# Kernel optimization log

Measured on AMD Instinct MI355X. Metric: run time of the kernel, lower is better.

Reference implementation:

```python
import jax, jax.numpy as jnp
import numpy as np

B = 524288  # batch
NQ = 4      # qubits -> 16-dim state vector


def _rx(t):
    c = jnp.cos(t / 2).astype(jnp.complex64)
    s = (-1j * jnp.sin(t / 2)).astype(jnp.complex64)
    return jnp.stack([jnp.stack([c, s], -1), jnp.stack([s, c], -1)], -2)


def _ry(t):
    c = jnp.cos(t / 2)
    s = jnp.sin(t / 2)
    return jnp.stack([jnp.stack([c, -s], -1), jnp.stack([s, c], -1)], -2).astype(jnp.complex64)


def _rz(t):
    em = jnp.exp(-0.5j * t).astype(jnp.complex64)
    ep = jnp.exp(0.5j * t).astype(jnp.complex64)
    z = jnp.zeros_like(em)
    return jnp.stack([jnp.stack([em, z], -1), jnp.stack([z, ep], -1)], -2)


def _apply(state, U, w):
    # state: [B,2,2,2,2]; wire w lives on axis w+1
    s = jnp.moveaxis(state, w + 1, 1)
    if U.ndim == 3:  # per-sample gate (encoder)
        s = jnp.einsum('bij,bj...->bi...', U, s)
    else:            # shared trainable gate
        s = jnp.einsum('ij,bj...->bi...', U, s)
    return jnp.moveaxis(s, 1, w + 1)


def _cnot(state, c, t):
    s = jnp.moveaxis(state, (c + 1, t + 1), (1, 2))
    s = jnp.stack([s[:, 0], s[:, 1, ::-1]], axis=1)  # flip target where control=1
    return jnp.moveaxis(s, (1, 2), (c + 1, t + 1))


def setup_inputs() -> dict:
    key = jax.random.key(0)
    k1, k2 = jax.random.split(key)
    inputs = jax.random.normal(k1, (B, 4), dtype=jnp.float32)
    theta = jax.random.normal(k2, (16,), dtype=jnp.float32)
    return {"inputs": inputs, "theta": theta}


def reference(inputs, theta):
    b = inputs.shape[0]
    state = jnp.zeros((b, 16), jnp.complex64).at[:, 0].set(1.0)
    state = state.reshape(b, 2, 2, 2, 2)
    # --- encoder: per-sample rotations rx(w0), ry(w1), rz(w2), rx(w3) ---
    state = _apply(state, _rx(inputs[:, 0]), 0)
    state = _apply(state, _ry(inputs[:, 1]), 1)
    state = _apply(state, _rz(inputs[:, 2]), 2)
    state = _apply(state, _rx(inputs[:, 3]), 3)
    # --- trainable 20-op layer (fixed representative sequence) ---
    k = 0
    for q in range(NQ):
        state = _apply(state, _rx(theta[k]), q); k += 1
        state = _apply(state, _ry(theta[k]), q); k += 1
        state = _apply(state, _rz(theta[k]), q); k += 1
    for (c, t) in [(0, 1), (1, 2), (2, 3), (3, 0)]:
        state = _cnot(state, c, t)
    for q in range(NQ):
        state = _apply(state, _rx(theta[k]), q); k += 1
    # --- MeasureAll(PauliZ): <Z_w> per wire ---
    flat = state.reshape(b, 16)
    probs = flat.real ** 2 + flat.imag ** 2  # [B,16]
    bits = (jnp.arange(16)[:, None] >> jnp.arange(NQ - 1, -1, -1)[None, :]) & 1  # [16,4], wire0=MSB
    sign = (1.0 - 2.0 * bits).astype(jnp.float32)
    expz = probs @ sign  # [B,4]
    return expz[:, :, None]  # unsqueeze(-1)
```

## Files before the change

### kernel.cpp

```cpp
#include <hip/hip_runtime.h>
#include <hip/hip_bf16.h>


__global__ __launch_bounds__(256) void qsim_kernel(
        const float* __restrict__ x,
        const float* __restrict__ theta,
        float* __restrict__ out,
        int n) {
    __shared__ __align__(16) float cst[40];
    int tid = threadIdx.x;
    if (tid < 4) {
        int q = tid;
        float a = theta[3*q], bb = theta[3*q+1], c = theta[3*q+2];
        float sa, ca, sb, cb, sc, cc;
        __sincosf(0.5f*a,  &sa, &ca);
        __sincosf(0.5f*bb, &sb, &cb);
        __sincosf(0.5f*c,  &sc, &cc);
        float m00r =  cb*ca, m00i =  sb*sa;
        float m01r = -sb*ca, m01i = -cb*sa;
        float m10r =  sb*ca, m10i = -cb*sa;
        float m11r =  cb*ca, m11i = -sb*sa;
        float* T = cst + 8*q;
        T[0] = cc*m00r + sc*m00i;  T[1] = cc*m00i - sc*m00r;
        T[2] = cc*m01r + sc*m01i;  T[3] = cc*m01i - sc*m01r;
        T[4] = cc*m10r - sc*m10i;  T[5] = cc*m10i + sc*m10r;
        T[6] = cc*m11r - sc*m11i;  T[7] = cc*m11i + sc*m11r;
        float sfq, cfq;
        __sincosf(theta[12+q], &sfq, &cfq);
        cst[32+q] = cfq;
        cst[36+q] = 2.0f*sfq;
    }
    __syncthreads();

    int b = blockIdx.x * 256 + tid;
    if (b >= n) return;

    float4 xv = ((const float4*)x)[b];

    float T[32];
    #pragma unroll
    for (int i = 0; i < 8; ++i) ((float4*)T)[i] = ((const float4*)cst)[i];
    float4 cf  = ((const float4*)cst)[8];
    float4 sf2 = ((const float4*)cst)[9];

    float s0 = __sinf(0.5f*xv.x), c0 = __cosf(0.5f*xv.x);
    float s1 = __sinf(0.5f*xv.y), c1 = __cosf(0.5f*xv.y);
    float s2 = __sinf(0.5f*xv.z), c2 = __cosf(0.5f*xv.z);
    float s3 = __sinf(0.5f*xv.w), c3 = __cosf(0.5f*xv.w);

    float var[4], vai[4], vbr[4], vbi[4];
    {
        const float* t = T + 0;
        var[0] = t[0]*c0 + t[3]*s0;  vai[0] = t[1]*c0 - t[2]*s0;
        vbr[0] = t[4]*c0 + t[7]*s0;  vbi[0] = t[5]*c0 - t[6]*s0;
    }
    {
        const float* t = T + 8;
        var[1] = t[0]*c1 + t[2]*s1;  vai[1] = t[1]*c1 + t[3]*s1;
        vbr[1] = t[4]*c1 + t[6]*s1;  vbi[1] = t[5]*c1 + t[7]*s1;
    }
    {
        const float* t = T + 16;
        var[2] = t[0]*c2 + t[1]*s2;  vai[2] = t[1]*c2 - t[0]*s2;
        vbr[2] = t[4]*c2 + t[5]*s2;  vbi[2] = t[5]*c2 - t[4]*s2;
    }
    {
        const float* t = T + 24;
        var[3] = t[0]*c3 + t[3]*s3;  vai[3] = t[1]*c3 - t[2]*s3;
        vbr[3] = t[4]*c3 + t[7]*s3;  vbi[3] = t[5]*c3 - t[6]*s3;
    }

    float u01r[4], u01i[4], u23r[4], u23i[4];
    #pragma unroll
    for (int i0 = 0; i0 < 2; ++i0) {
        float ar = i0 ? vbr[0] : var[0], ai = i0 ? vbi[0] : vai[0];
        #pragma unroll
        for (int i1 = 0; i1 < 2; ++i1) {
            float br = i1 ? vbr[1] : var[1], bi = i1 ? vbi[1] : vai[1];
            u01r[2*i0+i1] = ar*br - ai*bi;
            u01i[2*i0+i1] = ar*bi + ai*br;
        }
    }
    #pragma unroll
    for (int i2 = 0; i2 < 2; ++i2) {
        float ar = i2 ? vbr[2] : var[2], ai = i2 ? vbi[2] : vai[2];
        #pragma unroll
        for (int i3 = 0; i3 < 2; ++i3) {
            float br = i3 ? vbr[3] : var[3], bi = i3 ? vbi[3] : vai[3];
            u23r[2*i2+i3] = ar*br - ai*bi;
            u23i[2*i2+i3] = ar*bi + ai*br;
        }
    }
    float pr[16], pi[16];
    #pragma unroll
    for (int h = 0; h < 4; ++h)
        #pragma unroll
        for (int l = 0; l < 4; ++l) {
            pr[4*h+l] = u01r[h]*u23r[l] - u01i[h]*u23i[l];
            pi[4*h+l] = u01r[h]*u23i[l] + u01i[h]*u23r[l];
        }

    #define SWP(A,Bq) { float t_; t_=pr[A]; pr[A]=pr[Bq]; pr[Bq]=t_; \
                        t_=pi[A]; pi[A]=pi[Bq]; pi[Bq]=t_; }
    SWP(8,12)  SWP(9,13)  SWP(10,14) SWP(11,15)
    SWP(4,6)   SWP(5,7)   SWP(12,14) SWP(13,15)
    SWP(2,3)   SWP(6,7)   SWP(10,11) SWP(14,15)
    SWP(1,9)   SWP(3,11)  SWP(5,13)  SWP(7,15)
    #undef SWP

    float d[16];
    #pragma unroll
    for (int i = 0; i < 16; ++i) d[i] = pr[i]*pr[i] + pi[i]*pi[i];

    float s1a[8], d1[8];
    #pragma unroll
    for (int k = 0; k < 8; ++k) { s1a[k] = d[2*k]+d[2*k+1]; d1[k] = d[2*k]-d[2*k+1]; }
    float z3 = ((d1[0]+d1[1])+(d1[2]+d1[3])) + ((d1[4]+d1[5])+(d1[6]+d1[7]));
    float s2a[4], d2[4];
    #pragma unroll
    for (int k = 0; k < 4; ++k) { s2a[k] = s1a[2*k]+s1a[2*k+1]; d2[k] = s1a[2*k]-s1a[2*k+1]; }
    float z2 = (d2[0]+d2[1]) + (d2[2]+d2[3]);
    float s3a[2], d3[2];
    #pragma unroll
    for (int k = 0; k < 2; ++k) { s3a[k] = s2a[2*k]+s2a[2*k+1]; d3[k] = s2a[2*k]-s2a[2*k+1]; }
    float z1 = d3[0] + d3[1];
    float z0 = s3a[0] - s3a[1];

    float y[4];
    #pragma unroll
    for (int w = 0; w < 4; ++w) {
        int m = 8 >> w;
        float acc = 0.f;
        #pragma unroll
        for (int i = 0; i < 16; ++i)
            if (!(i & m)) acc += pr[i]*pi[i+m] - pi[i]*pr[i+m];
        y[w] = acc;
    }

    float4 o;
    o.x = cf.x*z0 + sf2.x*y[0];
    o.y = cf.y*z1 + sf2.y*y[1];
    o.z = cf.z*z2 + sf2.z*y[2];
    o.w = cf.w*z3 + sf2.w*y[3];
    ((float4*)out)[b] = o;
}

extern "C" void kernel_launch(void* const* d_in, const int* in_sizes, int n_in,
                              void* d_out, int out_size, void* d_ws, size_t ws_size,
                              hipStream_t stream) {
    const float* inputs = (const float*)d_in[0];
    const float* theta  = (const float*)d_in[1];
    float* out = (float*)d_out;
    int n = in_sizes[0] / 4;
    int blocks = (n + 255) / 256;
    qsim_kernel<<<blocks, 256, 0, stream>>>(inputs, theta, out, n);
}
```

Measured before the change: 67.22 us.

## Compute expectations analytically from per-qubit product-state Bloch components

```diff
diff --git a/kernel.cpp b/kernel.cpp
--- a/kernel.cpp
+++ b/kernel.cpp
@@ -1,5 +1,4 @@
 #include <hip/hip_runtime.h>
-#include <hip/hip_bf16.h>
 
 
 __global__ __launch_bounds__(256) void qsim_kernel(
@@ -20,15 +19,15 @@
         float m01r = -sb*ca, m01i = -cb*sa;
         float m10r =  sb*ca, m10i = -cb*sa;
         float m11r =  cb*ca, m11i = -sb*sa;
-        float* T = cst + 8*q;
-        T[0] = cc*m00r + sc*m00i;  T[1] = cc*m00i - sc*m00r;
-        T[2] = cc*m01r + sc*m01i;  T[3] = cc*m01i - sc*m01r;
-        T[4] = cc*m10r - sc*m10i;  T[5] = cc*m10i + sc*m10r;
-        T[6] = cc*m11r - sc*m11i;  T[7] = cc*m11i + sc*m11r;
+        float* Tq = cst + 8*q;
+        Tq[0] = cc*m00r + sc*m00i;  Tq[1] = cc*m00i - sc*m00r;
+        Tq[2] = cc*m01r + sc*m01i;  Tq[3] = cc*m01i - sc*m01r;
+        Tq[4] = cc*m10r - sc*m10i;  Tq[5] = cc*m10i + sc*m10r;
+        Tq[6] = cc*m11r - sc*m11i;  Tq[7] = cc*m11i + sc*m11r;
         float sfq, cfq;
         __sincosf(theta[12+q], &sfq, &cfq);
         cst[32+q] = cfq;
-        cst[36+q] = 2.0f*sfq;
+        cst[36+q] = (q == 3 ? -8.0f : 4.0f) * sfq;
     }
     __syncthreads();
 
@@ -40,8 +39,8 @@
     float T[32];
     #pragma unroll
     for (int i = 0; i < 8; ++i) ((float4*)T)[i] = ((const float4*)cst)[i];
-    float4 cf  = ((const float4*)cst)[8];
-    float4 sf2 = ((const float4*)cst)[9];
+    float4 cf = ((const float4*)cst)[8];
+    float4 sf = ((const float4*)cst)[9];
 
     float s0 = __sinf(0.5f*xv.x), c0 = __cosf(0.5f*xv.x);
     float s1 = __sinf(0.5f*xv.y), c1 = __cosf(0.5f*xv.y);
@@ -70,78 +69,23 @@
         vbr[3] = t[4]*c3 + t[7]*s3;  vbi[3] = t[5]*c3 - t[6]*s3;
     }
 
-    float u01r[4], u01i[4], u23r[4], u23i[4];
-    #pragma unroll
-    for (int i0 = 0; i0 < 2; ++i0) {
-        float ar = i0 ? vbr[0] : var[0], ai = i0 ? vbi[0] : vai[0];
-        #pragma unroll
-        for (int i1 = 0; i1 < 2; ++i1) {
-            float br = i1 ? vbr[1] : var[1], bi = i1 ? vbi[1] : vai[1];
-            u01r[2*i0+i1] = ar*br - ai*bi;
-            u01i[2*i0+i1] = ar*bi + ai*br;
-        }
-    }
-    #pragma unroll
-    for (int i2 = 0; i2 < 2; ++i2) {
-        float ar = i2 ? vbr[2] : var[2], ai = i2 ? vbi[2] : vai[2];
-        #pragma unroll
-        for (int i3 = 0; i3 < 2; ++i3) {
-            float br = i3 ? vbr[3] : var[3], bi = i3 ? vbi[3] : vai[3];
-            u23r[2*i2+i3] = ar*br - ai*bi;
-            u23i[2*i2+i3] = ar*bi + ai*br;
-        }
-    }
-    float pr[16], pi[16];
-    #pragma unroll
-    for (int h = 0; h < 4; ++h)
-        #pragma unroll
-        for (int l = 0; l < 4; ++l) {
-            pr[4*h+l] = u01r[h]*u23r[l] - u01i[h]*u23i[l];
-            pi[4*h+l] = u01r[h]*u23i[l] + u01i[h]*u23r[l];
-        }
-
-    #define SWP(A,Bq) { float t_; t_=pr[A]; pr[A]=pr[Bq]; pr[Bq]=t_; \
-                        t_=pi[A]; pi[A]=pi[Bq]; pi[Bq]=t_; }
-    SWP(8,12)  SWP(9,13)  SWP(10,14) SWP(11,15)
-    SWP(4,6)   SWP(5,7)   SWP(12,14) SWP(13,15)
-    SWP(2,3)   SWP(6,7)   SWP(10,11) SWP(14,15)
-    SWP(1,9)   SWP(3,11)  SWP(5,13)  SWP(7,15)
-    #undef SWP
-
-    float d[16];
-    #pragma unroll
-    for (int i = 0; i < 16; ++i) d[i] = pr[i]*pr[i] + pi[i]*pi[i];
-
-    float s1a[8], d1[8];
-    #pragma unroll
-    for (int k = 0; k < 8; ++k) { s1a[k] = d[2*k]+d[2*k+1]; d1[k] = d[2*k]-d[2*k+1]; }
-    float z3 = ((d1[0]+d1[1])+(d1[2]+d1[3])) + ((d1[4]+d1[5])+(d1[6]+d1[7]));
-    float s2a[4], d2[4];
-    #pragma unroll
-    for (int k = 0; k < 4; ++k) { s2a[k] = s1a[2*k]+s1a[2*k+1]; d2[k] = s1a[2*k]-s1a[2*k+1]; }
-    float z2 = (d2[0]+d2[1]) + (d2[2]+d2[3]);
-    float s3a[2], d3[2];
-    #pragma unroll
-    for (int k = 0; k < 2; ++k) { s3a[k] = s2a[2*k]+s2a[2*k+1]; d3[k] = s2a[2*k]-s2a[2*k+1]; }
-    float z1 = d3[0] + d3[1];
-    float z0 = s3a[0] - s3a[1];
-
-    float y[4];
+    float zq[4], Xq[4], Yq[4];
     #pragma unroll
     for (int w = 0; w < 4; ++w) {
-        int m = 8 >> w;
-        float acc = 0.f;
-        #pragma unroll
-        for (int i = 0; i < 16; ++i)
-            if (!(i & m)) acc += pr[i]*pi[i+m] - pi[i]*pr[i+m];
-        y[w] = acc;
+        float p0 = var[w]*var[w] + vai[w]*vai[w];
+        float p1 = vbr[w]*vbr[w] + vbi[w]*vbi[w];
+        zq[w] = p0 - p1;
+        Xq[w] = var[w]*vbr[w] + vai[w]*vbi[w];
+        Yq[w] = var[w]*vbi[w] - vai[w]*vbr[w];
     }
 
+    float z01 = zq[0]*zq[1];
+    float z23 = zq[2]*zq[3];
     float4 o;
-    o.x = cf.x*z0 + sf2.x*y[0];
-    o.y = cf.y*z1 + sf2.y*y[1];
-    o.z = cf.z*z2 + sf2.z*y[2];
-    o.w = cf.w*z3 + sf2.w*y[3];
+    o.x = (cf.x*zq[1] + sf.x*(Xq[0]*Yq[1])) * z23;
+    o.y = (cf.y*zq[1] + sf.y*(Yq[1]*Xq[2])) * zq[0];
+    o.z = (cf.z*zq[2] + sf.z*(Yq[2]*Xq[3])) * z01;
+    o.w = cf.w*(z01*z23) + sf.w*((Yq[0]*Yq[1])*(zq[2]*Yq[3]));
     ((float4*)out)[b] = o;
 }
 
```

After: 62.73 us. -6.7%, faster.
